# Performance work log

Measured on AMD Instinct MI355X. Metric: run time of the kernel, lower is better.

Reference implementation:

```python
import jax, jax.numpy as jnp
import numpy as np

B, L, DM, H, DH = 2, 2048, 1024, 4, 128
TOT = H * DH  # 512


def _dwconv(x, w, b, L):
    # x: (B,L,C), w: (C,1,4) depthwise, padding=3 then causal trim to L (matches Conv1d(padding=3)[...,:L])
    y = jax.lax.conv_general_dilated(x.transpose(0, 2, 1), w, (1,), [(3, 3)],
                                     dimension_numbers=('NCH', 'OIH', 'NCH'),
                                     feature_group_count=w.shape[0])
    y = y[..., :L] + b[None, :, None]
    return y.transpose(0, 2, 1)


def _l2norm(x):
    return x / jnp.maximum(jnp.linalg.norm(x, axis=-1, keepdims=True), 1e-12)


def setup_inputs() -> dict:
    key = jax.random.key(0)
    ks = jax.random.split(key, 16)
    s = 0.02
    return {
        'x': jax.random.normal(ks[0], (B, L, DM), jnp.float32),
        'state': jnp.zeros((B, H, DH, DH), jnp.float32),
        'Wq': jax.random.normal(ks[1], (TOT, DM), jnp.float32) * s,
        'Wk': jax.random.normal(ks[2], (TOT, DM), jnp.float32) * s,
        'Wv': jax.random.normal(ks[3], (2 * TOT, DM), jnp.float32) * s,
        'Wa': jax.random.normal(ks[4], (H, DM), jnp.float32) * s,
        'Wb': jax.random.normal(ks[5], (H, DM), jnp.float32) * s,
        'Wg': jax.random.normal(ks[6], (TOT, DM), jnp.float32) * s,
        'Wo': jax.random.normal(ks[7], (DM, TOT), jnp.float32) * s,
        'qcw': jax.random.normal(ks[8], (TOT, 1, 4), jnp.float32) * 0.1,
        'qcb': jnp.zeros((TOT,), jnp.float32),
        'kcw': jax.random.normal(ks[9], (TOT, 1, 4), jnp.float32) * 0.1,
        'kcb': jnp.zeros((TOT,), jnp.float32),
        'vcw': jax.random.normal(ks[10], (2 * TOT, 1, 4), jnp.float32) * 0.1,
        'vcb': jnp.zeros((2 * TOT,), jnp.float32),
        'ln_w': jnp.ones((TOT,), jnp.float32),
        'ln_b': jnp.zeros((TOT,), jnp.float32),
    }


def reference(x, state, Wq, Wk, Wv, Wa, Wb, Wg, Wo, qcw, qcb, kcw, kcb, vcw, vcb, ln_w, ln_b):
    Bn, Ln, _ = x.shape
    q = _dwconv(x @ Wq.T, qcw, qcb, Ln)
    k = _dwconv(x @ Wk.T, kcw, kcb, Ln)
    v = _dwconv(x @ Wv.T, vcw, vcb, Ln)
    # silu then L2-normalize over the FULL total_dim (before head split), as in the source
    q = _l2norm(jax.nn.silu(q))
    k = _l2norm(jax.nn.silu(k))
    v = jax.nn.silu(v)
    alpha = jax.nn.sigmoid(x @ Wa.T)  # (B,L,H)
    beta = jax.nn.sigmoid(x @ Wb.T)   # (B,L,H)
    q = q.reshape(Bn, Ln, H, DH)
    k = k.reshape(Bn, Ln, H, DH)
    v_main, v_gate = jnp.split(v, 2, axis=-1)
    v_main = v_main.reshape(Bn, Ln, H, DH)
    v_gate = v_gate.reshape(Bn, Ln, H, DH)

    def step(S, inp):
        q_t, k_t, v_t, a_t, b_t = inp  # (B,H,D),(B,H,D),(B,H,D),(B,H),(B,H)
        a = a_t[..., None, None]
        b = b_t[..., None, None]
        Sk = jnp.einsum('bhij,bhj->bhi', S, k_t)  # S @ k
        # S @ (alpha*(I - beta k k^T)) + beta v k^T, via rank-1 update
        S = a * (S - b * (Sk[..., :, None] * k_t[..., None, :])) \
            + b * (v_t[..., :, None] * k_t[..., None, :])
        o = jnp.einsum('bhij,bhj->bhi', S, q_t)
        return S, o

    xs = (q.transpose(1, 0, 2, 3), k.transpose(1, 0, 2, 3), v_main.transpose(1, 0, 2, 3),
          alpha.transpose(1, 0, 2), beta.transpose(1, 0, 2))
    final_state, outs = jax.lax.scan(step, state, xs)
    out = outs.transpose(1, 0, 2, 3)  # (B,L,H,D)

    out = (out * v_gate).reshape(Bn, Ln, TOT)
    out = out * jax.nn.silu(x @ Wg.T)
    mu = out.mean(-1, keepdims=True)
    var = jnp.mean((out - mu) ** 2, axis=-1, keepdims=True)
    out = (out - mu) * jax.lax.rsqrt(var + 1e-5) * ln_w + ln_b
    out = out @ Wo.T
    return out, final_state
```

## Files before the change

kernel.cpp:

```cpp
#include <hip/hip_runtime.h>
#include <hip/hip_bf16.h>

#define BQ    2
#define LQ    2048
#define DMQ   1024
#define HQ    4
#define DHQ   128
#define TOTQ  512
#define BLQ   4096
#define NPROJ 2688
#define KPROJ 1024
#define CT    64
#define NCH   32

typedef short bf16x8 __attribute__((ext_vector_type(8)));
typedef short s16x4  __attribute__((ext_vector_type(4)));
typedef float f32x4  __attribute__((ext_vector_type(4)));

#define MFMA16(a, b, c) __builtin_amdgcn_mfma_f32_16x16x32_bf16(a, b, c, 0, 0, 0)

__device__ __forceinline__ float siluf(float x) { return x / (1.f + __expf(-x)); }
__device__ __forceinline__ float sigf(float x)  { return 1.f / (1.f + __expf(-x)); }
__device__ __forceinline__ short bf16s(float x) {
  return __builtin_bit_cast(short, __float2bfloat16(x));
}
__device__ __forceinline__ float bfu2f(unsigned short u) {
  return __bfloat162float(__builtin_bit_cast(__hip_bfloat16, u));
}
__device__ __forceinline__ bf16x8 pack8(f32x4 a, f32x4 b) {
  bf16x8 r;
  r[0] = bf16s(a.x); r[1] = bf16s(a.y); r[2] = bf16s(a.z); r[3] = bf16s(a.w);
  r[4] = bf16s(b.x); r[5] = bf16s(b.y); r[6] = bf16s(b.z); r[7] = bf16s(b.w);
  return r;
}

__device__ __forceinline__ void gload_lds16(const void* g, void* l) {
  __builtin_amdgcn_global_load_lds(
      (__attribute__((address_space(1))) void*)(unsigned long long)g,
      (__attribute__((address_space(3))) void*)(unsigned int)(unsigned long long)l,
      16, 0, 0);
}

__global__ __launch_bounds__(256)
void cast_f32_bf16_kernel(const float* __restrict__ src, __hip_bfloat16* __restrict__ dst, int n4)
{
  int i = blockIdx.x * 256 + threadIdx.x;
  if (i < n4) {
    float4 v = ((const float4*)src)[i];
    __hip_bfloat16 o[4] = { __float2bfloat16(v.x), __float2bfloat16(v.y),
                            __float2bfloat16(v.z), __float2bfloat16(v.w) };
    *(ushort4*)((unsigned short*)dst + (size_t)i * 4) = *(ushort4*)o;
  }
}

__global__ __launch_bounds__(256)
void cast_wcat_kernel(const float* __restrict__ Wq, const float* __restrict__ Wk,
                      const float* __restrict__ Wv, const float* __restrict__ Wg,
                      const float* __restrict__ Wa, const float* __restrict__ Wb,
                      __hip_bfloat16* __restrict__ Wcat)
{
  int i4 = blockIdx.x * 256 + threadIdx.x;
  int row = i4 >> 8;
  int col = (i4 & 255) * 4;
  int idx = row * 1024 + col;
  float4 v;
  if      (row < 512)  v = *(const float4*)(Wq + idx);
  else if (row < 1024) v = *(const float4*)(Wk + idx - 512 * 1024);
  else if (row < 2048) v = *(const float4*)(Wv + idx - 1024 * 1024);
  else if (row < 2560) v = *(const float4*)(Wg + idx - 2048 * 1024);
  else if (row < 2564) v = *(const float4*)(Wa + (row - 2560) * 1024 + col);
  else if (row < 2568) v = *(const float4*)(Wb + (row - 2564) * 1024 + col);
  else                 v = make_float4(0.f, 0.f, 0.f, 0.f);
  __hip_bfloat16 o[4] = { __float2bfloat16(v.x), __float2bfloat16(v.y),
                          __float2bfloat16(v.z), __float2bfloat16(v.w) };
  *(ushort4*)((unsigned short*)Wcat + idx) = *(ushort4*)o;
}

template <typename TOUT>
__global__ __launch_bounds__(256)
void gemm_bt_kernel(const __hip_bfloat16* __restrict__ A,
                    const __hip_bfloat16* __restrict__ Bw,
                    TOUT* __restrict__ C, int M, int N, int K,
                    float* __restrict__ aux, int auxc0)
{
  __shared__ __hip_bfloat16 As[2 * 128 * 32];
  __shared__ __hip_bfloat16 Bs[2 * 128 * 32];
  const int tid  = threadIdx.x;
  const int lane = tid & 63;
  const int w    = tid >> 6;
  const int wm   = w >> 1, wn = w & 1;
  const int tm   = blockIdx.x, tn = blockIdx.y;
  const int lr   = lane & 15, lk = lane >> 4;

  f32x4 acc[4][4] = {};

  const int e0   = tid * 8;
  const int srow = e0 >> 5;
  const int scol = e0 & 31;
  const __hip_bfloat16* Ap = A  + (size_t)(tm * 128 + srow) * K + scol;
  const __hip_bfloat16* Bp = Bw + (size_t)(tn * 128 + srow) * K + scol;
  char* AsB  = (char*)As;
  char* BsB  = (char*)Bs;
  const size_t half = (size_t)64 * K;
  const int nk = K >> 5;

  {
    char* AsD = AsB + w * 1024;
    char* BsD = BsB + w * 1024;
    gload_lds16(Ap,        AsD);
    gload_lds16(Ap + half, AsD + 4096);
    gload_lds16(Bp,        BsD);
    gload_lds16(Bp + half, BsD + 4096);
  }
  __syncthreads();

  for (int it = 0; it < nk; ++it) {
    const int sel = it & 1;
    if (it + 1 < nk) {
      const int kk = (it + 1) * 32;
      char* AsD = AsB + ((sel ^ 1) * 8192) + w * 1024;
      char* BsD = BsB + ((sel ^ 1) * 8192) + w * 1024;
      gload_lds16(Ap + kk,        AsD);
      gload_lds16(Ap + half + kk, AsD + 4096);
      gload_lds16(Bp + kk,        BsD);
      gload_lds16(Bp + half + kk, BsD + 4096);
    }
    const char* AsR = AsB + sel * 8192;
    const char* BsR = BsB + sel * 8192;
    bf16x8 af[4], bfv[4];
#pragma unroll
    for (int m = 0; m < 4; ++m)
      af[m]  = *(const bf16x8*)(AsR + ((wm * 64 + m * 16 + lr) * 32 + lk * 8) * 2);
#pragma unroll
    for (int n = 0; n < 4; ++n)
      bfv[n] = *(const bf16x8*)(BsR + ((wn * 64 + n * 16 + lr) * 32 + lk * 8) * 2);
#pragma unroll
    for (int m = 0; m < 4; ++m)
#pragma unroll
      for (int n = 0; n < 4; ++n)
        acc[m][n] = MFMA16(af[m], bfv[n], acc[m][n]);
    __syncthreads();
  }

  const int crow0 = tm * 128 + wm * 64 + (lane >> 4) * 4;
  const int ccol0 = tn * 128 + wn * 64 + lr;
#pragma unroll
  for (int m = 0; m < 4; ++m)
#pragma unroll
    for (int n = 0; n < 4; ++n) {
      const int cc = ccol0 + n * 16;
#pragma unroll
      for (int j = 0; j < 4; ++j) {
        const float v = acc[m][n][j];
        const size_t row = (size_t)(crow0 + m * 16 + j);
        if constexpr (sizeof(TOUT) == 2)
          ((unsigned short*)C)[row * N + cc] = (unsigned short)bf16s(v);
        else
          C[row * N + cc] = v;
        if (aux && cc >= auxc0 && cc < auxc0 + 8)
          aux[row * 8 + (cc - auxc0)] = v;
      }
    }
}

__global__ __launch_bounds__(256)
void conv_act_kernel(const __hip_bfloat16* __restrict__ C, const float* __restrict__ abf,
                     const float* __restrict__ qcw, const float* __restrict__ qcb,
                     const float* __restrict__ kcw, const float* __restrict__ kcb,
                     const float* __restrict__ vcw, const float* __restrict__ vcb,
                     __hip_bfloat16* __restrict__ qh, __hip_bfloat16* __restrict__ kh,
                     __hip_bfloat16* __restrict__ vm, __hip_bfloat16* __restrict__ vg,
                     float* __restrict__ al, float* __restrict__ be)
{
  const int blk = blockIdx.x;
  const int bl0 = blk * 8;
  const int t0  = bl0 & (LQ - 1);
  const int tid = threadIdx.x;
  const unsigned short* Cu = (const unsigned short*)C;
  __shared__ float red[4][16];

  float2 qv[8], kv[8];
  float sq[8], sk[8];
#pragma unroll
  for (int t = 0; t < 8; ++t) { sq[t] = 0.f; sk[t] = 0.f; }

  {
    const int c0 = tid * 2;
    const float4 wqA = *(const float4*)(qcw + 4 * c0);
    const float4 wqB = *(const float4*)(qcw + 4 * c0 + 4);
    const float4 wkA = *(const float4*)(kcw + 4 * c0);
    const float4 wkB = *(const float4*)(kcw + 4 * c0 + 4);
    const float2 bq = *(const float2*)(qcb + c0);
    const float2 bk = *(const float2*)(kcb + c0);
    float2 wrq[11], wrk[11];
#pragma unroll
    for (int r = 0; r < 11; ++r) {
      const int tt = t0 - 3 + r;
      if (tt >= 0) {
        const unsigned short* Cr = Cu + (size_t)(bl0 - 3 + r) * NPROJ;
        const ushort2 aq = *(const ushort2*)(Cr + c0);
        const ushort2 ak = *(const ushort2*)(Cr + 512 + c0);
        wrq[r] = make_float2(bfu2f(aq.x), bfu2f(aq.y));
        wrk[r] = make_float2(bfu2f(ak.x), bfu2f(ak.y));
      } else {
        wrq[r] = make_float2(0.f, 0.f);
        wrk[r] = make_float2(0.f, 0.f);
      }
    }
#pragma unroll
    for (int t = 0; t < 8; ++t) {
      float aq0 = bq.x, aq1 = bq.y, ak0 = bk.x, ak1 = bk.y;
#pragma unroll
      for (int j = 0; j < 4; ++j) {
        aq0 = fmaf(((const float*)&wqA)[j], wrq[t + j].x, aq0);
        aq1 = fmaf(((const float*)&wqB)[j], wrq[t + j].y, aq1);
        ak0 = fmaf(((const float*)&wkA)[j], wrk[t + j].x, ak0);
        ak1 = fmaf(((const float*)&wkB)[j], wrk[t + j].y, ak1);
      }
      const float q0 = siluf(aq0), q1 = siluf(aq1);
      const float k0 = siluf(ak0), k1 = siluf(ak1);
      qv[t] = make_float2(q0, q1);
      kv[t] = make_float2(k0, k1);
      sq[t] = fmaf(q1, q1, fmaf(q0, q0, sq[t]));
      sk[t] = fmaf(k1, k1, fmaf(k0, k0, sk[t]));
    }
  }
#pragma unroll
  for (int m = 1; m < 64; m <<= 1) {
#pragma unroll
    for (int t = 0; t < 8; ++t) {
      sq[t] += __shfl_xor(sq[t], m);
      sk[t] += __shfl_xor(sk[t], m);
    }
  }
  {
    const int w = tid >> 6, lane = tid & 63;
    if (lane == 0) {
#pragma unroll
      for (int t = 0; t < 8; ++t) { red[w][t] = sq[t]; red[w][8 + t] = sk[t]; }
    }
  }
  __syncthreads();
  float rnq[8], rnk[8];
#pragma unroll
  for (int t = 0; t < 8; ++t) {
    const float SQ = red[0][t] + red[1][t] + red[2][t] + red[3][t];
    const float SK = red[0][8 + t] + red[1][8 + t] + red[2][8 + t] + red[3][8 + t];
    rnq[t] = 1.f / fmaxf(sqrtf(SQ), 1e-12f);
    rnk[t] = 1.f / fmaxf(sqrtf(SK), 1e-12f);
  }
  {
    const int c0 = tid * 2;
#pragma unroll
    for (int t = 0; t < 8; ++t) {
      ushort2 oq, ok;
      oq.x = (unsigned short)bf16s(qv[t].x * rnq[t]);
      oq.y = (unsigned short)bf16s(qv[t].y * rnq[t]);
      ok.x = (unsigned short)bf16s(kv[t].x * rnk[t]);
      ok.y = (unsigned short)bf16s(kv[t].y * rnk[t]);
      *(ushort2*)((unsigned short*)qh + (size_t)(bl0 + t) * 512 + c0) = oq;
      *(ushort2*)((unsigned short*)kh + (size_t)(bl0 + t) * 512 + c0) = ok;
    }
  }
  {
    const int cv = tid * 4;
    const float4 wv0 = *(const float4*)(vcw + 4 * cv);
    const float4 wv1 = *(const float4*)(vcw + 4 * cv + 4);
    const float4 wv2 = *(const float4*)(vcw + 4 * cv + 8);
    const float4 wv3 = *(const float4*)(vcw + 4 * cv + 12);
    const float4 bv4 = *(const float4*)(vcb + cv);
    float4 wr[11];
#pragma unroll
    for (int r = 0; r < 11; ++r) {
      const int tt = t0 - 3 + r;
      if (tt >= 0) {
        const ushort4 u = *(const ushort4*)(Cu + (size_t)(bl0 - 3 + r) * NPROJ + 1024 + cv);
        wr[r] = make_float4(bfu2f(u.x), bfu2f(u.y), bfu2f(u.z), bfu2f(u.w));
      } else {
        wr[r] = make_float4(0.f, 0.f, 0.f, 0.f);
      }
    }
#pragma unroll
    for (int t = 0; t < 8; ++t) {
      float a0 = bv4.x, a1 = bv4.y, a2 = bv4.z, a3 = bv4.w;
#pragma unroll
      for (int j = 0; j < 4; ++j) {
        a0 = fmaf(((const float*)&wv0)[j], ((const float*)&wr[t + j])[0], a0);
        a1 = fmaf(((const float*)&wv1)[j], ((const float*)&wr[t + j])[1], a1);
        a2 = fmaf(((const float*)&wv2)[j], ((const float*)&wr[t + j])[2], a2);
        a3 = fmaf(((const float*)&wv3)[j], ((const float*)&wr[t + j])[3], a3);
      }
      ushort4 o;
      o.x = (unsigned short)bf16s(siluf(a0));
      o.y = (unsigned short)bf16s(siluf(a1));
      o.z = (unsigned short)bf16s(siluf(a2));
      o.w = (unsigned short)bf16s(siluf(a3));
      if (cv < 512) *(ushort4*)((unsigned short*)vm + (size_t)(bl0 + t) * 512 + cv)         = o;
      else          *(ushort4*)((unsigned short*)vg + (size_t)(bl0 + t) * 512 + (cv - 512)) = o;
    }
  }
  if (tid < 64) {
    const int t = tid >> 3;
    const int k = tid & 7;
    const float v = abf[(size_t)(bl0 + t) * 8 + k];
    if (k < 4) al[(size_t)(bl0 + t) * 4 + k]       = sigf(v);
    else       be[(size_t)(bl0 + t) * 4 + (k - 4)] = sigf(v);
  }
}

__global__ __launch_bounds__(256)
void scan_phaseA_kernel(const __hip_bfloat16* __restrict__ qh, const __hip_bfloat16* __restrict__ kh,
                        const __hip_bfloat16* __restrict__ vm, const float* __restrict__ al,
                        const float* __restrict__ be,
                        short* __restrict__ WTB, short* __restrict__ ZB,
                        short* __restrict__ PHB, short* __restrict__ KTB,
                        float* __restrict__ GV, float* __restrict__ GC,
                        short* __restrict__ WTFB, short* __restrict__ ZFB)
{
  __shared__ char sm[83968];
  float* Xl = (float*)(sm);
  __hip_bfloat16* KBl = (__hip_bfloat16*)(sm);
  __hip_bfloat16* QBl = (__hip_bfloat16*)(sm + 17408);
  float* Ll  = (float*)(sm + 65536);
  float* dv  = (float*)(sm + 82944);
  float* bv  = (float*)(sm + 83200);
  float* gbv = (float*)(sm + 83456);
  float* fvs = (float*)(sm + 83712);

  const int cb = blockIdx.x;
  const int bh = cb & 7, c = cb >> 3;
  const int b = bh >> 2, h = bh & 3;
  const int tid = threadIdx.x;
  const int lane = tid & 63;
  const int w = tid >> 6;
  const int lr = lane & 15, lk = lane >> 4;
  const size_t rowbase = (size_t)(b * LQ + c * CT) * 512 + h * 128;

#pragma unroll
  for (int rep = 0; rep < 4; ++rep) {
    const int fid = tid + rep * 256;
    const int r = fid >> 4;
    const int cg = (fid & 15) * 8;
    *(bf16x8*)(KBl + r * 136 + cg) = *(const bf16x8*)(kh + rowbase + (size_t)r * 512 + cg);
    *(bf16x8*)(QBl + r * 136 + cg) = *(const bf16x8*)(qh + rowbase + (size_t)r * 512 + cg);
  }
  if (w == 0) {
    float la = __logf(al[(size_t)(b * LQ + c * CT + lane) * 4 + h]);
    const float bb = be[(size_t)(b * LQ + c * CT + lane) * 4 + h];
#pragma unroll
    for (int off = 1; off < 64; off <<= 1) {
      const float tv = __shfl_up(la, off, 64);
      if (lane >= off) la += tv;
    }
    const float d63 = __shfl(la, 63, 64);
    dv[lane] = la; bv[lane] = bb; gbv[lane] = bb * __expf(la);
    fvs[lane] = __expf(d63 - la);
    GV[cb * 64 + lane] = __expf(la);
    if (lane == 0) GC[cb] = __expf(d63);
  }
  __syncthreads();

  f32x4 aG[4] = {}, aP[4] = {};
#pragma unroll
  for (int ks = 0; ks < 4; ++ks) {
    bf16x8 bk[4];
#pragma unroll
    for (int nt = 0; nt < 4; ++nt)
      bk[nt] = *(const bf16x8*)(KBl + (nt * 16 + lr) * 136 + ks * 32 + lk * 8);
    const bf16x8 ak = *(const bf16x8*)(KBl + (w * 16 + lr) * 136 + ks * 32 + lk * 8);
    const bf16x8 aq = *(const bf16x8*)(QBl + (w * 16 + lr) * 136 + ks * 32 + lk * 8);
#pragma unroll
    for (int nt = 0; nt < 4; ++nt) {
      aG[nt] = MFMA16(ak, bk[nt], aG[nt]);
      aP[nt] = MFMA16(aq, bk[nt], aP[nt]);
    }
  }
#pragma unroll
  for (int nt = 0; nt < 4; ++nt)
#pragma unroll
    for (int jj = 0; jj < 4; ++jj) {
      const int t = w * 16 + lk * 4 + jj;
      const int s = nt * 16 + lr;
      const float eg = __expf(dv[t] - dv[s]);
      Ll[t * 68 + s] = (t > s) ? bv[t] * eg * aG[nt][jj] : 0.f;
      PHB[(size_t)cb * 4096 + t * 64 + s] = (s <= t) ? bf16s(eg * aP[nt][jj]) : (short)0;
    }
  __syncthreads();

  const int j = tid;
  const __hip_bfloat16* src = (j < 128) ? kh : vm;
  const __hip_bfloat16* xp = src + rowbase + (j & 127);
  float* XlC = Xl + j;
  short* dstN = (j < 128) ? (WTB + (size_t)cb * 8192 + j)
                          : (ZB  + (size_t)cb * 8192 + (j - 128));
  short* dstT = (j < 128) ? (WTFB + (size_t)cb * 8192 + (size_t)j * 64)
                          : (ZFB  + (size_t)cb * 8192 + (size_t)(j - 128) * 64);

  for (int r = 0; r < 4; ++r) {
    float u[16];
#pragma unroll
    for (int i = 0; i < 16; ++i) {
      const int t = r * 16 + i;
      u[i] = __bfloat162float(xp[(size_t)t * 512]) * ((j < 128) ? gbv[t] : bv[t]);
    }
    for (int sc = 0; sc < r; ++sc) {
      float xs[16];
#pragma unroll
      for (int k = 0; k < 16; ++k) xs[k] = XlC[(sc * 16 + k) * 256];
#pragma unroll
      for (int i = 0; i < 16; ++i) {
        const float* lrow = Ll + (r * 16 + i) * 68 + sc * 16;
        const f32x4 l0 = *(const f32x4*)(lrow);
        const f32x4 l1 = *(const f32x4*)(lrow + 4);
        const f32x4 l2 = *(const f32x4*)(lrow + 8);
        const f32x4 l3 = *(const f32x4*)(lrow + 12);
        f32x4 acc = {};
        acc.x = fmaf(l0.x, xs[0],  acc.x); acc.y = fmaf(l0.y, xs[1],  acc.y);
        acc.z = fmaf(l0.z, xs[2],  acc.z); acc.w = fmaf(l0.w, xs[3],  acc.w);
        acc.x = fmaf(l1.x, xs[4],  acc.x); acc.y = fmaf(l1.y, xs[5],  acc.y);
        acc.z = fmaf(l1.z, xs[6],  acc.z); acc.w = fmaf(l1.w, xs[7],  acc.w);
        acc.x = fmaf(l2.x, xs[8],  acc.x); acc.y = fmaf(l2.y, xs[9],  acc.y);
        acc.z = fmaf(l2.z, xs[10], acc.z); acc.w = fmaf(l2.w, xs[11], acc.w);
        acc.x = fmaf(l3.x, xs[12], acc.x); acc.y = fmaf(l3.y, xs[13], acc.y);
        acc.z = fmaf(l3.z, xs[14], acc.z); acc.w = fmaf(l3.w, xs[15], acc.w);
        u[i] -= (acc.x + acc.y) + (acc.z + acc.w);
      }
    }
#pragma unroll
    for (int i = 1; i < 16; ++i) {
      const float* lrow = Ll + (r * 16 + i) * 68 + r * 16;
      f32x4 acc = {};
#pragma unroll
      for (int k4 = 0; k4 < 4; ++k4) {
        if (k4 * 4 < i) {
          const f32x4 lv = *(const f32x4*)(lrow + k4 * 4);
          acc.x = fmaf(lv.x, u[k4 * 4 + 0], acc.x);
          acc.y = fmaf(lv.y, u[k4 * 4 + 1], acc.y);
          acc.z = fmaf(lv.z, u[k4 * 4 + 2], acc.z);
          acc.w = fmaf(lv.w, u[k4 * 4 + 3], acc.w);
        }
      }
      u[i] -= (acc.x + acc.y) + (acc.z + acc.w);
    }
    if (r < 3) {
#pragma unroll
      for (int i = 0; i < 16; ++i) XlC[(r * 16 + i) * 256] = u[i];
    }
#pragma unroll
    for (int i = 0; i < 16; ++i)
      dstN[(r * 16 + i) * 128] = bf16s(u[i]);
#pragma unroll
    for (int s4 = 0; s4 < 4; ++s4) {
      s16x4 p;
#pragma unroll
      for (int e = 0; e < 4; ++e)
        p[e] = bf16s(fvs[r * 16 + s4 * 4 + e] * u[s4 * 4 + e]);
      *(s16x4*)(dstT + r * 16 + s4 * 4) = p;
    }
  }

  if (tid < 128) {
    const short* kp2 = (const short*)kh + rowbase + tid;
#pragma unroll
    for (int s4 = 0; s4 < 16; ++s4) {
      s16x4 pk;
#pragma unroll
      for (int e = 0; e < 4; ++e)
        pk[e] = kp2[(size_t)(s4 * 4 + e) * 512];
      *(s16x4*)(KTB + (size_t)cb * 8192 + tid * 64 + s4 * 4) = pk;
    }
  }
}

__global__ __launch_bounds__(256)
void scan_transition_kernel(const short* __restrict__ WTFB, const short* __restrict__ ZFB,
                            const short* __restrict__ KTB, const float* __restrict__ GC,
                            short* __restrict__ TRB, float* __restrict__ BF)
{
  const int cb = blockIdx.x;
  const int tid = threadIdx.x, lane = tid & 63, w = tid >> 6;
  const int lr = lane & 15, lk = lane >> 4;
  const float gc = GC[cb];

  {
    f32x4 acc[2][8] = {};
#pragma unroll
    for (int ks = 0; ks < 2; ++ks) {
      bf16x8 a0 = *(const bf16x8*)(KTB + (size_t)cb * 8192 + (w * 32 + lr) * 64 + ks * 32 + lk * 8);
      bf16x8 a1 = *(const bf16x8*)(KTB + (size_t)cb * 8192 + (w * 32 + 16 + lr) * 64 + ks * 32 + lk * 8);
#pragma unroll
      for (int nt = 0; nt < 8; ++nt) {
        const bf16x8 bm = *(const bf16x8*)(WTFB + (size_t)cb * 8192 + (nt * 16 + lr) * 64 + ks * 32 + lk * 8);
        acc[0][nt] = MFMA16(a0, bm, acc[0][nt]);
        acc[1][nt] = MFMA16(a1, bm, acc[1][nt]);
      }
    }
#pragma unroll
    for (int mt = 0; mt < 2; ++mt)
#pragma unroll
      for (int nt = 0; nt < 8; ++nt)
#pragma unroll
        for (int jj = 0; jj < 4; ++jj) {
          const int jr = w * 32 + mt * 16 + lk * 4 + jj;
          const int m  = nt * 16 + lr;
          const float v = ((jr == m) ? gc : 0.f) - acc[mt][nt][jj];
          TRB[(size_t)cb * 16384 + jr * 128 + m] = bf16s(v);
        }
  }
  {
    f32x4 acc[2][8] = {};
#pragma unroll
    for (int ks = 0; ks < 2; ++ks) {
      bf16x8 a0 = *(const bf16x8*)(ZFB + (size_t)cb * 8192 + (w * 32 + lr) * 64 + ks * 32 + lk * 8);
      bf16x8 a1 = *(const bf16x8*)(ZFB + (size_t)cb * 8192 + (w * 32 + 16 + lr) * 64 + ks * 32 + lk * 8);
#pragma unroll
      for (int nt = 0; nt < 8; ++nt) {
        const bf16x8 bj = *(const bf16x8*)(KTB + (size_t)cb * 8192 + (nt * 16 + lr) * 64 + ks * 32 + lk * 8);
        acc[0][nt] = MFMA16(a0, bj, acc[0][nt]);
        acc[1][nt] = MFMA16(a1, bj, acc[1][nt]);
      }
    }
#pragma unroll
    for (int mt = 0; mt < 2; ++mt)
#pragma unroll
      for (int nt = 0; nt < 8; ++nt)
#pragma unroll
        for (int jj = 0; jj < 4; ++jj) {
          const int ir = w * 32 + mt * 16 + lk * 4 + jj;
          const int jc = nt * 16 + lr;
          BF[(size_t)cb * 16384 + ir * 128 + jc] = acc[mt][nt][jj];
        }
  }
}

#define L2_PREFETCH(BT, BA, CC) do {                                               \
  const int cbn_ = (CC) * 8 + bh;                                                  \
  _Pragma("unroll") for (int nt = 0; nt < 2; ++nt) {                               \
    _Pragma("unroll") for (int ks = 0; ks < 4; ++ks)                               \
      BT[nt][ks] = *(const bf16x8*)(TRB + (size_t)cbn_ * 16384 +                   \
                                    (w * 32 + nt * 16 + lr) * 128 + ks * 32 + lk * 8); \
    _Pragma("unroll") for (int jj = 0; jj < 4; ++jj)                               \
      BA[nt][jj] = BF[(size_t)cbn_ * 16384 + (r0 + lk * 4 + jj) * 128 +            \
                      w * 32 + nt * 16 + lr];                                      \
  }                                                                                \
} while (0)

#define L2_STEP(BT, BA, CC, PBT, PBA) do {                                         \
  const int cb_ = (CC) * 8 + bh;                                                   \
  { const int idx = tid * 8, r = idx >> 7, jc = idx & 127;                         \
    f32x4 s0 = *(const f32x4*)&Scur[r * 132 + jc];                                 \
    f32x4 s1 = *(const f32x4*)&Scur[r * 132 + jc + 4];                             \
    *(bf16x8*)(SALL + (size_t)cb_ * 16384 + (r0 + r) * 128 + jc) = pack8(s0, s1); }\
  bf16x8 af[4];                                                                    \
  _Pragma("unroll") for (int ks = 0; ks < 4; ++ks)                                 \
    af[ks] = pack8(*(const f32x4*)&Scur[lr * 132 + ks * 32 + lk * 8],              \
                   *(const f32x4*)&Scur[lr * 132 + ks * 32 + lk * 8 + 4]);         \
  if ((CC) < 31) L2_PREFETCH(PBT, PBA, (CC) + 1);                                  \
  f32x4 acc0 = {}, acc1 = {};                                                      \
  _Pragma("unroll") for (int ks = 0; ks < 4; ++ks) {                               \
    acc0 = MFMA16(af[ks], BT[0][ks], acc0);                                        \
    acc1 = MFMA16(af[ks], BT[1][ks], acc1);                                        \
  }                                                                                \
  _Pragma("unroll") for (int jj = 0; jj < 4; ++jj) {                               \
    Snxt[(lk * 4 + jj) * 132 + w * 32 + lr]      = acc0[jj] + BA[0][jj];           \
    Snxt[(lk * 4 + jj) * 132 + w * 32 + 16 + lr] = acc1[jj] + BA[1][jj];           \
  }                                                                                \
  __syncthreads();                                                                 \
  { float* t_ = Scur; Scur = Snxt; Snxt = t_; }                                    \
} while (0)

__global__ __launch_bounds__(256)
void scan_state_kernel(const short* __restrict__ TRB, const float* __restrict__ BF,
                       const float* __restrict__ st0, short* __restrict__ SALL,
                       float* __restrict__ stout)
{
  __shared__ float Sl[2 * 16 * 132];
  const int bid = blockIdx.x;
  const int bh = bid & 7, slab = bid >> 3;
  const int r0 = slab * 16;
  const int tid = threadIdx.x, lane = tid & 63, w = tid >> 6;
  const int lr = lane & 15, lk = lane >> 4;

  float* Scur = Sl;
  float* Snxt = Sl + 16 * 132;

  {
    const int idx = tid * 8, r = idx >> 7, jc = idx & 127;
    const float* sp = st0 + ((size_t)bh * 128 + r0 + r) * 128 + jc;
    *(f32x4*)&Scur[r * 132 + jc]     = *(const f32x4*)sp;
    *(f32x4*)&Scur[r * 132 + jc + 4] = *(const f32x4*)(sp + 4);
  }
  bf16x8 btA[2][4], btB[2][4];
  float  baA[2][4], baB[2][4];
  L2_PREFETCH(btA, baA, 0);
  __syncthreads();

  for (int c2 = 0; c2 < 16; ++c2) {
    L2_STEP(btA, baA, 2 * c2,     btB, baB);
    L2_STEP(btB, baB, 2 * c2 + 1, btA, baA);
  }

  {
    const int idx = tid * 8, r = idx >> 7, jc = idx & 127;
    float* sp = stout + ((size_t)bh * 128 + r0 + r) * 128 + jc;
    *(f32x4*)sp       = *(const f32x4*)&Scur[r * 132 + jc];
    *(f32x4*)(sp + 4) = *(const f32x4*)&Scur[r * 132 + jc + 4];
  }
}

__global__ __launch_bounds__(512)
void scan_output_kernel(const __hip_bfloat16* __restrict__ qh,
                        const short* __restrict__ WTB, const __hip_bfloat16* __restrict__ ZB,
                        const short* __restrict__ PHB, const float* __restrict__ GV,
                        const short* __restrict__ SALL, float* __restrict__ obuf)
{
  __shared__ short Ut[128 * 72];
  const int cb = blockIdx.x;
  const int bh = cb & 7, c = cb >> 3;
  const int b = bh >> 2, h = bh & 3;
  const int tid = threadIdx.x, lane = tid & 63, w = tid >> 6;
  const int lr = lane & 15, lk = lane >> 4;
  const int r0 = (w & 3) * 16;

  f32x4 Y[8] = {};
#pragma unroll
  for (int ks = 0; ks < 4; ++ks) {
    bf16x8 af;
    if (w < 4) {
      af = *(const bf16x8*)(qh + ((size_t)(b * LQ + c * CT) + r0 + lr) * 512 + h * 128 + ks * 32 + lk * 8);
    } else {
      af = *(const bf16x8*)(WTB + (size_t)cb * 8192 + (r0 + lr) * 128 + ks * 32 + lk * 8);
    }
#pragma unroll
    for (int nt = 0; nt < 8; ++nt) {
      const bf16x8 bs = *(const bf16x8*)(SALL + (size_t)cb * 16384 + (nt * 16 + lr) * 128 + ks * 32 + lk * 8);
      Y[nt] = MFMA16(af, bs, Y[nt]);
    }
  }
  if (w >= 4) {
#pragma unroll
    for (int nt = 0; nt < 8; ++nt) {
      const int i = nt * 16 + lr;
      s16x4 up;
#pragma unroll
      for (int jj = 0; jj < 4; ++jj) {
        const int s = r0 + lk * 4 + jj;
        const float z = __bfloat162float(ZB[(size_t)cb * 8192 + s * 128 + i]);
        up[jj] = bf16s(z - Y[nt][jj]);
      }
      *(s16x4*)&Ut[i * 72 + r0 + lk * 4] = up;
    }
  }
  __syncthreads();
  if (w < 4) {
    f32x4 P2[8] = {};
#pragma unroll
    for (int ks = 0; ks < 2; ++ks) {
      const bf16x8 ap = *(const bf16x8*)(PHB + (size_t)cb * 4096 + (r0 + lr) * 64 + ks * 32 + lk * 8);
#pragma unroll
      for (int nt = 0; nt < 8; ++nt) {
        const bf16x8 bu = *(const bf16x8*)&Ut[(nt * 16 + lr) * 72 + ks * 32 + lk * 8];
        P2[nt] = MFMA16(ap, bu, P2[nt]);
      }
    }
    float gvv[4];
#pragma unroll
    for (int jj = 0; jj < 4; ++jj) gvv[jj] = GV[cb * 64 + r0 + lk * 4 + jj];
#pragma unroll
    for (int nt = 0; nt < 8; ++nt) {
      const int i = nt * 16 + lr;
#pragma unroll
      for (int jj = 0; jj < 4; ++jj) {
        const int t = r0 + lk * 4 + jj;
        obuf[((size_t)(b * LQ + c * CT) + t) * 512 + h * 128 + i] =
            gvv[jj] * Y[nt][jj] + P2[nt][jj];
      }
    }
  }
}

__global__ __launch_bounds__(256)
void gate_ln_kernel(const float* __restrict__ obuf, const __hip_bfloat16* __restrict__ vg,
                    const __hip_bfloat16* __restrict__ C, const float* __restrict__ lnw,
                    const float* __restrict__ lnb, __hip_bfloat16* __restrict__ lno)
{
  const int bl = blockIdx.x, tid = threadIdx.x;
  const int c0 = tid * 2;
  __shared__ float red[8];
  const float2 ov = *(const float2*)(obuf + (size_t)bl * 512 + c0);
  const ushort2 gvu = *(const ushort2*)((const unsigned short*)vg + (size_t)bl * 512 + c0);
  const ushort2 ggu = *(const ushort2*)((const unsigned short*)C + (size_t)bl * NPROJ + 2048 + c0);
  const float v0 = ov.x * bfu2f(gvu.x) * siluf(bfu2f(ggu.x));
  const float v1 = ov.y * bfu2f(gvu.y) * siluf(bfu2f(ggu.y));
  float s = v0 + v1;
  float s2 = fmaf(v1, v1, v0 * v0);
  float2 pr = make_float2(s, s2);
#pragma unroll
  for (int m = 1; m < 64; m <<= 1) { pr.x += __shfl_xor(pr.x, m); pr.y += __shfl_xor(pr.y, m); }
  if ((tid & 63) == 0) { red[(tid >> 6) * 2] = pr.x; red[(tid >> 6) * 2 + 1] = pr.y; }
  __syncthreads();
  const float S  = red[0] + red[2] + red[4] + red[6];
  const float S2 = red[1] + red[3] + red[5] + red[7];
  const float mu  = S * (1.f / 512.f);
  const float var = S2 * (1.f / 512.f) - mu * mu;
  const float rs  = rsqrtf(var + 1e-5f);
  const float2 lw = *(const float2*)(lnw + c0);
  const float2 lb = *(const float2*)(lnb + c0);
  __hip_bfloat16 o[2] = {
    __float2bfloat16(fmaf((v0 - mu) * rs, lw.x, lb.x)),
    __float2bfloat16(fmaf((v1 - mu) * rs, lw.y, lb.y)) };
  *(ushort2*)((unsigned short*)lno + (size_t)bl * 512 + c0) = *(ushort2*)o;
}

extern "C" void kernel_launch(void* const* d_in, const int* in_sizes, int n_in,
                              void* d_out, int out_size, void* d_ws, size_t ws_size,
                              hipStream_t stream)
{
  (void)in_sizes; (void)n_in; (void)out_size; (void)ws_size;
  const float* x    = (const float*)d_in[0];
  const float* st0  = (const float*)d_in[1];
  const float* Wq   = (const float*)d_in[2];
  const float* Wk   = (const float*)d_in[3];
  const float* Wv   = (const float*)d_in[4];
  const float* Wa   = (const float*)d_in[5];
  const float* Wb   = (const float*)d_in[6];
  const float* Wg   = (const float*)d_in[7];
  const float* Wo   = (const float*)d_in[8];
  const float* qcw  = (const float*)d_in[9];
  const float* qcb  = (const float*)d_in[10];
  const float* kcw  = (const float*)d_in[11];
  const float* kcb  = (const float*)d_in[12];
  const float* vcw  = (const float*)d_in[13];
  const float* vcb  = (const float*)d_in[14];
  const float* lnw  = (const float*)d_in[15];
  const float* lnb  = (const float*)d_in[16];
  float* out = (float*)d_out;

  char* ws = (char*)d_ws;
  __hip_bfloat16* XB   = (__hip_bfloat16*)(ws + 0);
  __hip_bfloat16* LNO  = (__hip_bfloat16*)(ws + 0);
  short*          WTFB = (short*)(ws + 0);
  short*          WTB  = (short*)(ws + 4194304);
  __hip_bfloat16* WCAT = (__hip_bfloat16*)(ws + 8388608);
  __hip_bfloat16* WOB  = (__hip_bfloat16*)(ws + 13893632);
  __hip_bfloat16* CBUFH = (__hip_bfloat16*)(ws + 14942208);
  __hip_bfloat16* QH   = (__hip_bfloat16*)(ws + 58982400);
  __hip_bfloat16* KH   = (__hip_bfloat16*)(ws + 67371008);
  float* BF   = (float*)(ws + 67371008);
  __hip_bfloat16* VM   = (__hip_bfloat16*)(ws + 75759616);
  __hip_bfloat16* VG   = (__hip_bfloat16*)(ws + 84148224);
  float* AL   = (float*)(ws + 92536832);
  float* BE   = (float*)(ws + 92602368);
  float* OBUF = (float*)(ws + 92667904);
  short* TRB  = (short*)(ws + 92667904);
  short* KTB  = (short*)(ws + 101056512);
  short* PHB  = (short*)(ws + 105250816);
  short* ZB   = (short*)(ws + 107347968);
  float* GV   = (float*)(ws + 111542272);
  float* GC   = (float*)(ws + 111673344);
  short* ZFB  = (short*)(ws + 111674368);
  short* SALL = (short*)(ws + 115868672);
  float* ABF  = (float*)(ws + 124257280);

  cast_f32_bf16_kernel<<<4096, 256, 0, stream>>>(x,  XB,  1048576);
  cast_f32_bf16_kernel<<<512,  256, 0, stream>>>(Wo, WOB, 131072);
  cast_wcat_kernel<<<2688, 256, 0, stream>>>(Wq, Wk, Wv, Wg, Wa, Wb, WCAT);

  gemm_bt_kernel<__hip_bfloat16><<<dim3(32, 21), 256, 0, stream>>>(
      XB, WCAT, CBUFH, BLQ, NPROJ, KPROJ, ABF, 2560);

  conv_act_kernel<<<512, 256, 0, stream>>>(CBUFH, ABF, qcw, qcb, kcw, kcb, vcw, vcb,
                                           QH, KH, VM, VG, AL, BE);

  scan_phaseA_kernel<<<256, 256, 0, stream>>>(QH, KH, VM, AL, BE,
                                              WTB, ZB, PHB, KTB, GV, GC, WTFB, ZFB);

  scan_transition_kernel<<<256, 256, 0, stream>>>(WTFB, ZFB, KTB, GC, TRB, BF);

  scan_state_kernel<<<64, 256, 0, stream>>>(TRB, BF, st0, SALL, out + 4194304);

  scan_output_kernel<<<256, 512, 0, stream>>>(QH, WTB, (const __hip_bfloat16*)ZB,
                                              PHB, GV, SALL, OBUF);

  gate_ln_kernel<<<BLQ, 256, 0, stream>>>(OBUF, VG, CBUFH, lnw, lnb, LNO);

  gemm_bt_kernel<float><<<dim3(32, 8), 256, 0, stream>>>(
      LNO, WOB, out, BLQ, DMQ, TOTQ, nullptr, 0);
}
```

Before: 159.3 us.

## Fuse scan transition kernel into phase A via shared-memory staging

Merges the chunk transition-matrix computation into the phase-A scan kernel. K^T, the scaled W and the Z tiles are kept in padded LDS instead of being written to global memory and re-read by a separate kernel. This removes one kernel launch and the global round trip of three intermediate buffers. LDS per block grows to about 136 KB, which lowers occupancy to one block per CU. BF is moved to a new workspace offset so it does not alias KH, which the fused kernel still reads.

```diff
diff --git a/kernel.cpp b/kernel.cpp
--- a/kernel.cpp
+++ b/kernel.cpp
@@ -313,11 +313,10 @@
                         const __hip_bfloat16* __restrict__ vm, const float* __restrict__ al,
                         const float* __restrict__ be,
                         short* __restrict__ WTB, short* __restrict__ ZB,
-                        short* __restrict__ PHB, short* __restrict__ KTB,
-                        float* __restrict__ GV, float* __restrict__ GC,
-                        short* __restrict__ WTFB, short* __restrict__ ZFB)
-{
-  __shared__ char sm[83968];
+                        short* __restrict__ PHB, float* __restrict__ GV,
+                        short* __restrict__ TRB, float* __restrict__ BF)
+{
+  __shared__ char sm[136192];
   float* Xl = (float*)(sm);
   __hip_bfloat16* KBl = (__hip_bfloat16*)(sm);
   __hip_bfloat16* QBl = (__hip_bfloat16*)(sm + 17408);
@@ -326,6 +325,9 @@
   float* bv  = (float*)(sm + 83200);
   float* gbv = (float*)(sm + 83456);
   float* fvs = (float*)(sm + 83712);
+  short* KTl  = (short*)(sm + 83968);
+  short* WTFl = (short*)(sm + 101376);
+  short* ZFl  = (short*)(sm + 118784);
 
   const int cb = blockIdx.x;
   const int bh = cb & 7, c = cb >> 3;
@@ -352,11 +354,10 @@
       const float tv = __shfl_up(la, off, 64);
       if (lane >= off) la += tv;
     }
+    dv[lane] = la; bv[lane] = bb; gbv[lane] = bb * __expf(la);
     const float d63 = __shfl(la, 63, 64);
-    dv[lane] = la; bv[lane] = bb; gbv[lane] = bb * __expf(la);
     fvs[lane] = __expf(d63 - la);
     GV[cb * 64 + lane] = __expf(la);
-    if (lane == 0) GC[cb] = __expf(d63);
   }
   __syncthreads();
 
@@ -385,6 +386,17 @@
       Ll[t * 68 + s] = (t > s) ? bv[t] * eg * aG[nt][jj] : 0.f;
       PHB[(size_t)cb * 4096 + t * 64 + s] = (s <= t) ? bf16s(eg * aP[nt][jj]) : (short)0;
     }
+  if (tid < 128) {
+    const short* Kbs = (const short*)KBl;
+#pragma unroll
+    for (int s4 = 0; s4 < 16; ++s4) {
+      s16x4 pk;
+#pragma unroll
+      for (int e = 0; e < 4; ++e)
+        pk[e] = Kbs[(s4 * 4 + e) * 136 + tid];
+      *(s16x4*)(KTl + tid * 68 + s4 * 4) = pk;
+    }
+  }
   __syncthreads();
 
   const int j = tid;
@@ -393,8 +405,8 @@
   float* XlC = Xl + j;
   short* dstN = (j < 128) ? (WTB + (size_t)cb * 8192 + j)
                           : (ZB  + (size_t)cb * 8192 + (j - 128));
-  short* dstT = (j < 128) ? (WTFB + (size_t)cb * 8192 + (size_t)j * 64)
-                          : (ZFB  + (size_t)cb * 8192 + (size_t)(j - 128) * 64);
+  short* dstT = (j < 128) ? (WTFl + j * 68)
+                          : (ZFl  + (j - 128) * 68);
 
   for (int r = 0; r < 4; ++r) {
     float u[16];
@@ -458,39 +470,18 @@
       *(s16x4*)(dstT + r * 16 + s4 * 4) = p;
     }
   }
-
-  if (tid < 128) {
-    const short* kp2 = (const short*)kh + rowbase + tid;
-#pragma unroll
-    for (int s4 = 0; s4 < 16; ++s4) {
-      s16x4 pk;
-#pragma unroll
-      for (int e = 0; e < 4; ++e)
-        pk[e] = kp2[(size_t)(s4 * 4 + e) * 512];
-      *(s16x4*)(KTB + (size_t)cb * 8192 + tid * 64 + s4 * 4) = pk;
-    }
-  }
-}
-
-__global__ __launch_bounds__(256)
-void scan_transition_kernel(const short* __restrict__ WTFB, const short* __restrict__ ZFB,
-                            const short* __restrict__ KTB, const float* __restrict__ GC,
-                            short* __restrict__ TRB, float* __restrict__ BF)
-{
-  const int cb = blockIdx.x;
-  const int tid = threadIdx.x, lane = tid & 63, w = tid >> 6;
-  const int lr = lane & 15, lk = lane >> 4;
-  const float gc = GC[cb];
-
+  __syncthreads();
+
+  const float gc = __expf(dv[63]);
   {
     f32x4 acc[2][8] = {};
 #pragma unroll
     for (int ks = 0; ks < 2; ++ks) {
-      bf16x8 a0 = *(const bf16x8*)(KTB + (size_t)cb * 8192 + (w * 32 + lr) * 64 + ks * 32 + lk * 8);
-      bf16x8 a1 = *(const bf16x8*)(KTB + (size_t)cb * 8192 + (w * 32 + 16 + lr) * 64 + ks * 32 + lk * 8);
+      const bf16x8 a0 = *(const bf16x8*)(KTl + (w * 32 + lr) * 68 + ks * 32 + lk * 8);
+      const bf16x8 a1 = *(const bf16x8*)(KTl + (w * 32 + 16 + lr) * 68 + ks * 32 + lk * 8);
 #pragma unroll
       for (int nt = 0; nt < 8; ++nt) {
-        const bf16x8 bm = *(const bf16x8*)(WTFB + (size_t)cb * 8192 + (nt * 16 + lr) * 64 + ks * 32 + lk * 8);
+        const bf16x8 bm = *(const bf16x8*)(WTFl + (nt * 16 + lr) * 68 + ks * 32 + lk * 8);
         acc[0][nt] = MFMA16(a0, bm, acc[0][nt]);
         acc[1][nt] = MFMA16(a1, bm, acc[1][nt]);
       }
@@ -511,11 +502,11 @@
     f32x4 acc[2][8] = {};
 #pragma unroll
     for (int ks = 0; ks < 2; ++ks) {
-      bf16x8 a0 = *(const bf16x8*)(ZFB + (size_t)cb * 8192 + (w * 32 + lr) * 64 + ks * 32 + lk * 8);
-      bf16x8 a1 = *(const bf16x8*)(ZFB + (size_t)cb * 8192 + (w * 32 + 16 + lr) * 64 + ks * 32 + lk * 8);
+      const bf16x8 a0 = *(const bf16x8*)(ZFl + (w * 32 + lr) * 68 + ks * 32 + lk * 8);
+      const bf16x8 a1 = *(const bf16x8*)(ZFl + (w * 32 + 16 + lr) * 68 + ks * 32 + lk * 8);
 #pragma unroll
       for (int nt = 0; nt < 8; ++nt) {
-        const bf16x8 bj = *(const bf16x8*)(KTB + (size_t)cb * 8192 + (nt * 16 + lr) * 64 + ks * 32 + lk * 8);
+        const bf16x8 bj = *(const bf16x8*)(KTl + (nt * 16 + lr) * 68 + ks * 32 + lk * 8);
         acc[0][nt] = MFMA16(a0, bj, acc[0][nt]);
         acc[1][nt] = MFMA16(a1, bj, acc[1][nt]);
       }
@@ -739,28 +730,24 @@
   char* ws = (char*)d_ws;
   __hip_bfloat16* XB   = (__hip_bfloat16*)(ws + 0);
   __hip_bfloat16* LNO  = (__hip_bfloat16*)(ws + 0);
-  short*          WTFB = (short*)(ws + 0);
   short*          WTB  = (short*)(ws + 4194304);
   __hip_bfloat16* WCAT = (__hip_bfloat16*)(ws + 8388608);
   __hip_bfloat16* WOB  = (__hip_bfloat16*)(ws + 13893632);
   __hip_bfloat16* CBUFH = (__hip_bfloat16*)(ws + 14942208);
   __hip_bfloat16* QH   = (__hip_bfloat16*)(ws + 58982400);
   __hip_bfloat16* KH   = (__hip_bfloat16*)(ws + 67371008);
-  float* BF   = (float*)(ws + 67371008);
   __hip_bfloat16* VM   = (__hip_bfloat16*)(ws + 75759616);
   __hip_bfloat16* VG   = (__hip_bfloat16*)(ws + 84148224);
   float* AL   = (float*)(ws + 92536832);
   float* BE   = (float*)(ws + 92602368);
   float* OBUF = (float*)(ws + 92667904);
   short* TRB  = (short*)(ws + 92667904);
-  short* KTB  = (short*)(ws + 101056512);
   short* PHB  = (short*)(ws + 105250816);
   short* ZB   = (short*)(ws + 107347968);
   float* GV   = (float*)(ws + 111542272);
-  float* GC   = (float*)(ws + 111673344);
-  short* ZFB  = (short*)(ws + 111674368);
   short* SALL = (short*)(ws + 115868672);
   float* ABF  = (float*)(ws + 124257280);
+  float* BF   = (float*)(ws + 124388352);
 
   cast_f32_bf16_kernel<<<4096, 256, 0, stream>>>(x,  XB,  1048576);
   cast_f32_bf16_kernel<<<512,  256, 0, stream>>>(Wo, WOB, 131072);
@@ -773,9 +760,7 @@
                                            QH, KH, VM, VG, AL, BE);
 
   scan_phaseA_kernel<<<256, 256, 0, stream>>>(QH, KH, VM, AL, BE,
-                                              WTB, ZB, PHB, KTB, GV, GC, WTFB, ZFB);
-
-  scan_transition_kernel<<<256, 256, 0, stream>>>(WTFB, ZFB, KTB, GC, TRB, BF);
+                                              WTB, ZB, PHB, GV, TRB, BF);
 
   scan_state_kernel<<<64, 256, 0, stream>>>(TRB, BF, st0, SALL, out + 4194304);
 
```

Measured after the change: 151.4 us. 5.0% less time.
